# Performance work log

Hardware: AMD Instinct MI355X
Metric: run time of the kernel (lower is better)

## Reference

```python
import jax, jax.numpy as jnp
import numpy as np

D_MODEL = 1024
N_HEADS = 16
HEAD_DIM = D_MODEL // N_HEADS
ROPE_BASE = 10000.0


def setup_inputs() -> dict:
    key = jax.random.key(0)
    ks = jax.random.split(key, 5)
    B, S = 2, 2048
    x = jax.random.normal(ks[0], (B, S, D_MODEL), dtype=jnp.float32)
    scale = 1.0 / np.sqrt(D_MODEL)
    Wq = jax.random.normal(ks[1], (D_MODEL, D_MODEL), dtype=jnp.float32) * scale
    Wk = jax.random.normal(ks[2], (D_MODEL, D_MODEL), dtype=jnp.float32) * scale
    Wv = jax.random.normal(ks[3], (D_MODEL, D_MODEL), dtype=jnp.float32) * scale
    Wo = jax.random.normal(ks[4], (D_MODEL, D_MODEL), dtype=jnp.float32) * scale
    return {"x": x, "Wq": Wq, "Wk": Wk, "Wv": Wv, "Wo": Wo}


def _rope_cos_sin(seq_len, dtype):
    # inv_freq over half the head dim, duplicated (cat[freqs, freqs])
    inv_freq = 1.0 / (ROPE_BASE ** (jnp.arange(0, HEAD_DIM, 2, dtype=jnp.float32) / HEAD_DIM))
    t = jnp.arange(seq_len, dtype=jnp.float32)
    freqs = jnp.outer(t, inv_freq)                 # [S, HD/2]
    emb = jnp.concatenate([freqs, freqs], axis=-1)  # [S, HD]
    return jnp.cos(emb).astype(dtype), jnp.sin(emb).astype(dtype)


def _rotate_half(v):
    v1, v2 = jnp.split(v, 2, axis=-1)
    return jnp.concatenate([-v2, v1], axis=-1)


def reference(x, Wq, Wk, Wv, Wo):
    B, S, _ = x.shape
    # torch Linear: y = x @ W.T  (weights stored [out, in])
    def proj(W):
        y = jnp.einsum('bsd,ed->bse', x, W)
        return y.reshape(B, S, N_HEADS, HEAD_DIM).transpose(0, 2, 1, 3)  # [B,H,S,HD]
    q, k, v = proj(Wq), proj(Wk), proj(Wv)

    cos, sin = _rope_cos_sin(S, x.dtype)  # [S, HD]
    cos = cos[None, None]                 # [1,1,S,HD]
    sin = sin[None, None]
    q = q * cos + _rotate_half(q) * sin
    k = k * cos + _rotate_half(k) * sin

    scale = 1.0 / np.sqrt(HEAD_DIM)
    scores = jnp.einsum('bhqd,bhkd->bhqk', q, k) * scale  # [B,H,S,S]
    causal = jnp.triu(jnp.ones((S, S), dtype=bool), k=1)
    scores = jnp.where(causal, jnp.finfo(scores.dtype).min, scores)
    attn = jax.nn.softmax(scores, axis=-1)
    out = jnp.einsum('bhqk,bhkd->bhqd', attn, v)          # [B,H,S,HD]
    out = out.transpose(0, 2, 1, 3).reshape(B, S, D_MODEL)
    return jnp.einsum('bsd,ed->bse', out, Wo)
```

## Files before the change

### kernel.cpp

```cpp
#include <hip/hip_runtime.h>

typedef unsigned short u16;
typedef __attribute__((ext_vector_type(8))) short short8;
typedef __attribute__((ext_vector_type(4))) float floatx4;

#define D_MODEL 1024
#define NHEADS 16
#define HD 64
#define BATCH 2
#define SEQ 2048
#define MROWS (BATCH * SEQ)

static __device__ __forceinline__ u16 f2bf(float f) {
  unsigned int u = __float_as_uint(f);
  u += 0x7fffu + ((u >> 16) & 1u);
  return (u16)(u >> 16);
}

__global__ void cvt_all(const float* __restrict__ x, const float* __restrict__ wq,
                        const float* __restrict__ wk, const float* __restrict__ wv,
                        const float* __restrict__ wo, u16* __restrict__ xb,
                        u16* __restrict__ wqkvb, u16* __restrict__ wob) {
  const int i = blockIdx.x * 256 + threadIdx.x;
  const int chunk = i >> 18;
  const float* src;
  u16* dst;
  int loc;
  switch (chunk) {
    case 0: case 1: case 2: case 3: src = x;  dst = xb;              loc = i;              break;
    case 4:                          src = wq; dst = wqkvb;           loc = i - (4 << 18); break;
    case 5:                          src = wk; dst = wqkvb + 1048576; loc = i - (5 << 18); break;
    case 6:                          src = wv; dst = wqkvb + 2097152; loc = i - (6 << 18); break;
    default:                         src = wo; dst = wob;             loc = i - (7 << 18); break;
  }
  const float4 v = ((const float4*)src)[loc];
  ushort4 o;
  o.x = f2bf(v.x); o.y = f2bf(v.y); o.z = f2bf(v.z); o.w = f2bf(v.w);
  ((ushort4*)dst)[loc] = o;
}

__global__ __launch_bounds__(256) void gemm_qkv(
    const u16* __restrict__ A, const u16* __restrict__ B,
    u16* __restrict__ qb, u16* __restrict__ kb, u16* __restrict__ vb, int K) {
  __shared__ u16 As[2][128 * 32];
  __shared__ u16 Bs[2][128 * 32];
  const int t = threadIdx.x;
  const int lane = t & 63;
  const int wv = t >> 6;
  const int wr = wv >> 1, wc = wv & 1;
  const int m0 = blockIdx.y * 128, n0 = blockIdx.x * 128;
  const int qd = lane >> 4, lr = lane & 15;
  const int arow = lane >> 2;
  const int acol = (lane & 3) * 8;

  floatx4 acc[4][4];
#pragma unroll
  for (int i = 0; i < 4; ++i)
#pragma unroll
    for (int j = 0; j < 4; ++j) acc[i][j] = (floatx4){0.f, 0.f, 0.f, 0.f};

  for (int kt = 0; kt < K; kt += 64) {
    __syncthreads();
#pragma unroll
    for (int kh = 0; kh < 2; ++kh) {
#pragma unroll
      for (int i = 0; i < 2; ++i) {
        const int seg = wv * 2 + i;
        const u16* ga = &A[(size_t)(m0 + seg * 16 + arow) * K + kt + kh * 32 + acol];
        const u16* gb = &B[(size_t)(n0 + seg * 16 + arow) * K + kt + kh * 32 + acol];
        __builtin_amdgcn_global_load_lds(
            (const __attribute__((address_space(1))) void*)ga,
            (__attribute__((address_space(3))) void*)&As[kh][seg * 512], 16, 0, 0);
        __builtin_amdgcn_global_load_lds(
            (const __attribute__((address_space(1))) void*)gb,
            (__attribute__((address_space(3))) void*)&Bs[kh][seg * 512], 16, 0, 0);
      }
    }
    __syncthreads();

#pragma unroll
    for (int kh = 0; kh < 2; ++kh) {
      short8 af[4], bfr[4];
#pragma unroll
      for (int i = 0; i < 4; ++i)
        af[i] = *(const short8*)&As[kh][(wr * 64 + i * 16 + lr) * 32 + qd * 8];
#pragma unroll
      for (int j = 0; j < 4; ++j)
        bfr[j] = *(const short8*)&Bs[kh][(wc * 64 + j * 16 + lr) * 32 + qd * 8];
#pragma unroll
      for (int i = 0; i < 4; ++i)
#pragma unroll
        for (int j = 0; j < 4; ++j)
          acc[i][j] = __builtin_amdgcn_mfma_f32_16x16x32_bf16(af[i], bfr[j], acc[i][j], 0, 0, 0);
    }
  }

  const int tn = n0 >> 10;
  if (tn == 2) {
#pragma unroll
    for (int i = 0; i < 4; ++i) {
      const int mb = m0 + wr * 64 + i * 16 + qd * 4;
      const int b = mb >> 11, s = mb & 2047;
#pragma unroll
      for (int j = 0; j < 4; ++j) {
        const int nn = (n0 + wc * 64 + j * 16 + lr) & 1023;
        const int h = nn >> 6, d = nn & 63;
        ushort4 o;
        o.x = f2bf(acc[i][j][0]); o.y = f2bf(acc[i][j][1]);
        o.z = f2bf(acc[i][j][2]); o.w = f2bf(acc[i][j][3]);
        *(ushort4*)&vb[((size_t)(b * NHEADS + h) * HD + d) * SEQ + s] = o;
      }
    }
  } else {
    u16* dst = (tn == 0) ? qb : kb;
    const float qs = (tn == 0) ? 0.18033688011112042f : 1.0f;
    const int h = ((n0 & 1023) >> 6) + wc;
    const float inv0 = __builtin_exp2f(-(float)lr * 0.4152410118609203f);
    const float inv1 = __builtin_exp2f(-(float)(lr + 16) * 0.4152410118609203f);
#pragma unroll
    for (int i = 0; i < 4; ++i) {
      const int mb = m0 + wr * 64 + i * 16 + qd * 4;
      const int b = mb >> 11;
      const size_t rowbase = (size_t)(b * NHEADS + h) * SEQ;
#pragma unroll
      for (int r = 0; r < 4; ++r) {
        const int sq = (mb + r) & 2047;
        float s0, c0, s1, c1;
        __sincosf((float)sq * inv0, &s0, &c0);
        __sincosf((float)sq * inv1, &s1, &c1);
#pragma unroll
        for (int j = 0; j < 4; ++j) {
          const float v = acc[i][j][r];
          const float pv = acc[i][j ^ 2][r];
          const float cc = (j & 1) ? c1 : c0;
          const float ss = (j & 1) ? s1 : s0;
          const float res = (v * cc + ((j < 2) ? -pv : pv) * ss) * qs;
          dst[(rowbase + sq) * HD + j * 16 + lr] = f2bf(res);
        }
      }
    }
  }
}

__global__ __launch_bounds__(256) void gemm_out(
    const u16* __restrict__ A, const u16* __restrict__ B, float* __restrict__ fo,
    int N, int K) {
  __shared__ u16 As[2][64 * 32];
  __shared__ u16 Bs[2][64 * 32];
  const int t = threadIdx.x;
  const int lane = t & 63, wv = t >> 6;
  const int m0 = blockIdx.y * 64, n0 = blockIdx.x * 64;
  const int qd = lane >> 4, lr = lane & 15;
  const int arow = lane >> 2;
  const int acol = (lane & 3) * 8;

  floatx4 acc[4];
#pragma unroll
  for (int j = 0; j < 4; ++j) acc[j] = (floatx4){0.f, 0.f, 0.f, 0.f};

  for (int kt = 0; kt < K; kt += 64) {
    __syncthreads();
#pragma unroll
    for (int kh = 0; kh < 2; ++kh) {
      const u16* ga = &A[(size_t)(m0 + wv * 16 + arow) * K + kt + kh * 32 + acol];
      const u16* gb = &B[(size_t)(n0 + wv * 16 + arow) * K + kt + kh * 32 + acol];
      __builtin_amdgcn_global_load_lds(
          (const __attribute__((address_space(1))) void*)ga,
          (__attribute__((address_space(3))) void*)&As[kh][wv * 512], 16, 0, 0);
      __builtin_amdgcn_global_load_lds(
          (const __attribute__((address_space(1))) void*)gb,
          (__attribute__((address_space(3))) void*)&Bs[kh][wv * 512], 16, 0, 0);
    }
    __syncthreads();

#pragma unroll
    for (int kh = 0; kh < 2; ++kh) {
      const short8 af = *(const short8*)&As[kh][(wv * 16 + lr) * 32 + qd * 8];
#pragma unroll
      for (int j = 0; j < 4; ++j) {
        const short8 bfr = *(const short8*)&Bs[kh][(j * 16 + lr) * 32 + qd * 8];
        acc[j] = __builtin_amdgcn_mfma_f32_16x16x32_bf16(af, bfr, acc[j], 0, 0, 0);
      }
    }
  }
#pragma unroll
  for (int j = 0; j < 4; ++j)
#pragma unroll
    for (int r = 0; r < 4; ++r)
      fo[(size_t)(m0 + wv * 16 + qd * 4 + r) * N + n0 + j * 16 + lr] = acc[j][r];
}

__global__ __launch_bounds__(256, 2) void flash_mfma(
    const u16* __restrict__ Q, const u16* __restrict__ Kg,
    const u16* __restrict__ Vg, u16* __restrict__ O) {
  __shared__ u16 Ks[2][2][64 * 32];
  __shared__ u16 Vs[2][2][64 * 32];
  __shared__ u16 Ps[4][2][16][72];
  const int t = threadIdx.x;
  const int lane = t & 63, wv = t >> 6;
  const int lr = lane & 15, qd = lane >> 4;
  const int bh = blockIdx.x;
  const int y = (int)blockIdx.y;
  const int c = (y < 8) ? (15 - y) : (y - 8);
  const int nsteps = 2 * c + 2;
  const int q0w = c * 128 + wv * 32;
  const size_t baseQK = (size_t)bh * SEQ * HD;
  const size_t baseV = (size_t)bh * HD * SEQ;
  const int b = bh >> 4, h = bh & 15;
  const int srow = lane >> 2;
  const int scol = (lane & 3) * 8;

  auto stage = [&](int buf, int k0) {
    const int hh = wv & 1;
    if (wv < 2) {
#pragma unroll
      for (int seg = 0; seg < 4; ++seg) {
        const u16* g = &Kg[baseQK + (size_t)(k0 + seg * 16 + srow) * HD + hh * 32 + scol];
        __builtin_amdgcn_global_load_lds(
            (const __attribute__((address_space(1))) void*)g,
            (__attribute__((address_space(3))) void*)&Ks[buf][hh][seg * 512], 16, 0, 0);
      }
    } else {
#pragma unroll
      for (int seg = 0; seg < 4; ++seg) {
        const u16* g = &Vg[baseV + (size_t)(seg * 16 + srow) * SEQ + k0 + hh * 32 + scol];
        __builtin_amdgcn_global_load_lds(
            (const __attribute__((address_space(1))) void*)g,
            (__attribute__((address_space(3))) void*)&Vs[buf][hh][seg * 512], 16, 0, 0);
      }
    }
  };

  short8 qf[2][2];
#pragma unroll
  for (int i = 0; i < 2; ++i)
#pragma unroll
    for (int s = 0; s < 2; ++s)
      qf[i][s] = *(const short8*)&Q[baseQK + (size_t)(q0w + i * 16 + lr) * HD + s * 32 + qd * 8];

  float l_i[2] = {0.f, 0.f};
  floatx4 oacc[2][4];
#pragma unroll
  for (int i = 0; i < 2; ++i)
#pragma unroll
    for (int dj = 0; dj < 4; ++dj) oacc[i][dj] = (floatx4){0.f, 0.f, 0.f, 0.f};

  stage(0, 0);

  for (int kt = 0; kt < nsteps; ++kt) {
    __syncthreads();
    if (kt + 1 < nsteps) stage((kt + 1) & 1, (kt + 1) * 64);
    const int k0 = kt * 64;
    if (k0 > q0w + 31) continue;
    const int buf = kt & 1;

    short8 kf[2][4], vf[2][4];
#pragma unroll
    for (int s = 0; s < 2; ++s)
#pragma unroll
      for (int jj = 0; jj < 4; ++jj)
        kf[s][jj] = *(const short8*)&Ks[buf][s][(jj * 16 + lr) * 32 + qd * 8];
#pragma unroll
    for (int s = 0; s < 2; ++s)
#pragma unroll
      for (int dj = 0; dj < 4; ++dj)
        vf[s][dj] = *(const short8*)&Vs[buf][s][(dj * 16 + lr) * 32 + qd * 8];

    floatx4 sv[2][4];
#pragma unroll
    for (int i = 0; i < 2; ++i)
#pragma unroll
      for (int jj = 0; jj < 4; ++jj) sv[i][jj] = (floatx4){0.f, 0.f, 0.f, 0.f};
#pragma unroll
    for (int s = 0; s < 2; ++s)
#pragma unroll
      for (int jj = 0; jj < 4; ++jj) {
        sv[1][jj] = __builtin_amdgcn_mfma_f32_16x16x32_bf16(kf[s][jj], qf[1][s], sv[1][jj], 0, 0, 0);
        sv[0][jj] = __builtin_amdgcn_mfma_f32_16x16x32_bf16(kf[s][jj], qf[0][s], sv[0][jj], 0, 0, 0);
      }

#pragma unroll
    for (int i = 0; i < 2; ++i) {
      const int dq = (q0w + i * 16) - k0;
      if (dq < 63) {
#pragma unroll
        for (int jj = 0; jj < 4; ++jj)
#pragma unroll
          for (int r = 0; r < 4; ++r)
            if (jj * 16 + qd * 4 + r > dq + lr) sv[i][jj][r] = -1e30f;
      }
      float rs = 0.f;
#pragma unroll
      for (int jj = 0; jj < 4; ++jj) {
        const float p0 = __builtin_exp2f(sv[i][jj][0]);
        const float p1 = __builtin_exp2f(sv[i][jj][1]);
        const float p2 = __builtin_exp2f(sv[i][jj][2]);
        const float p3 = __builtin_exp2f(sv[i][jj][3]);
        rs += (p0 + p1) + (p2 + p3);
        uint2 pk;
        pk.x = __builtin_amdgcn_perm(__float_as_uint(p1), __float_as_uint(p0), 0x07060302);
        pk.y = __builtin_amdgcn_perm(__float_as_uint(p3), __float_as_uint(p2), 0x07060302);
        *(uint2*)&Ps[wv][i][lr][jj * 16 + qd * 4] = pk;
      }
      l_i[i] += rs;
    }

#pragma unroll
    for (int i = 0; i < 2; ++i) {
      const short8 pf0 = *(const short8*)&Ps[wv][i][lr][qd * 8];
      const short8 pf1 = *(const short8*)&Ps[wv][i][lr][32 + qd * 8];
#pragma unroll
      for (int dj = 0; dj < 4; ++dj)
        oacc[i][dj] = __builtin_amdgcn_mfma_f32_16x16x32_bf16(pf0, vf[0][dj], oacc[i][dj], 0, 0, 0);
#pragma unroll
      for (int dj = 0; dj < 4; ++dj)
        oacc[i][dj] = __builtin_amdgcn_mfma_f32_16x16x32_bf16(pf1, vf[1][dj], oacc[i][dj], 0, 0, 0);
    }
  }

#pragma unroll
  for (int i = 0; i < 2; ++i) {
    float lf = l_i[i];
    lf += __shfl_xor(lf, 16, 64);
    lf += __shfl_xor(lf, 32, 64);
#pragma unroll
    for (int r = 0; r < 4; ++r) {
      const float linv = 1.f / __shfl(lf, qd * 4 + r, 64);
      const int q = q0w + i * 16 + qd * 4 + r;
#pragma unroll
      for (int dj = 0; dj < 4; ++dj)
        O[(size_t)(b * SEQ + q) * D_MODEL + h * HD + dj * 16 + lr] = f2bf(oacc[i][dj][r] * linv);
    }
  }
}

extern "C" void kernel_launch(void* const* d_in, const int* in_sizes, int n_in,
                              void* d_out, int out_size, void* d_ws, size_t ws_size,
                              hipStream_t stream) {
  const float* x  = (const float*)d_in[0];
  const float* Wq = (const float*)d_in[1];
  const float* Wk = (const float*)d_in[2];
  const float* Wv = (const float*)d_in[3];
  const float* Wo = (const float*)d_in[4];
  float* out = (float*)d_out;

  u16* xb = (u16*)d_ws;
  u16* wqkv = xb + 4194304;
  u16* wo = wqkv + 3145728;
  u16* qb = wo + 1048576;
  u16* kb = qb + 4194304;
  u16* vb = kb + 4194304;
  u16* ow = vb + 4194304;

  cvt_all<<<8192, 256, 0, stream>>>(x, Wq, Wk, Wv, Wo, xb, wqkv, wo);
  gemm_qkv<<<dim3(24, 32), 256, 0, stream>>>(xb, wqkv, qb, kb, vb, 1024);
  flash_mfma<<<dim3(32, 16), 256, 0, stream>>>(qb, kb, vb, ow);
  gemm_out<<<dim3(16, 64), 256, 0, stream>>>(ow, wo, out, 1024, 1024);
}
```

Measured before the change: 180.6 us.

## Split flash attention block across 8 waves with 16 query rows each

The attention kernel now runs 512 threads per block (8 waves), and each wave handles 16 query rows instead of 32. K/V staging is spread so every wave issues one K and one V async load per tile. The aim is more wave-level parallelism and latency hiding per CU, with fewer registers per wave. The cost is that each K/V fragment loaded from LDS now feeds half as many MFMAs, so LDS read traffic per FLOP doubles, and there are more threads per barrier.

```diff
diff --git a/kernel.cpp b/kernel.cpp
--- a/kernel.cpp
+++ b/kernel.cpp
@@ -190,12 +190,12 @@
       fo[(size_t)(m0 + wv * 16 + qd * 4 + r) * N + n0 + j * 16 + lr] = acc[j][r];
 }
 
-__global__ __launch_bounds__(256, 2) void flash_mfma(
+__global__ __launch_bounds__(512, 4) void flash_mfma(
     const u16* __restrict__ Q, const u16* __restrict__ Kg,
     const u16* __restrict__ Vg, u16* __restrict__ O) {
   __shared__ u16 Ks[2][2][64 * 32];
   __shared__ u16 Vs[2][2][64 * 32];
-  __shared__ u16 Ps[4][2][16][72];
+  __shared__ u16 Ps[8][16][72];
   const int t = threadIdx.x;
   const int lane = t & 63, wv = t >> 6;
   const int lr = lane & 15, qd = lane >> 4;
@@ -203,47 +203,35 @@
   const int y = (int)blockIdx.y;
   const int c = (y < 8) ? (15 - y) : (y - 8);
   const int nsteps = 2 * c + 2;
-  const int q0w = c * 128 + wv * 32;
+  const int q0w = c * 128 + wv * 16;
   const size_t baseQK = (size_t)bh * SEQ * HD;
   const size_t baseV = (size_t)bh * HD * SEQ;
   const int b = bh >> 4, h = bh & 15;
   const int srow = lane >> 2;
   const int scol = (lane & 3) * 8;
+  const int shh = (wv >> 2) & 1;
+  const int sseg = wv & 3;
 
   auto stage = [&](int buf, int k0) {
-    const int hh = wv & 1;
-    if (wv < 2) {
-#pragma unroll
-      for (int seg = 0; seg < 4; ++seg) {
-        const u16* g = &Kg[baseQK + (size_t)(k0 + seg * 16 + srow) * HD + hh * 32 + scol];
-        __builtin_amdgcn_global_load_lds(
-            (const __attribute__((address_space(1))) void*)g,
-            (__attribute__((address_space(3))) void*)&Ks[buf][hh][seg * 512], 16, 0, 0);
-      }
-    } else {
-#pragma unroll
-      for (int seg = 0; seg < 4; ++seg) {
-        const u16* g = &Vg[baseV + (size_t)(seg * 16 + srow) * SEQ + k0 + hh * 32 + scol];
-        __builtin_amdgcn_global_load_lds(
-            (const __attribute__((address_space(1))) void*)g,
-            (__attribute__((address_space(3))) void*)&Vs[buf][hh][seg * 512], 16, 0, 0);
-      }
-    }
+    const u16* gk = &Kg[baseQK + (size_t)(k0 + sseg * 16 + srow) * HD + shh * 32 + scol];
+    __builtin_amdgcn_global_load_lds(
+        (const __attribute__((address_space(1))) void*)gk,
+        (__attribute__((address_space(3))) void*)&Ks[buf][shh][sseg * 512], 16, 0, 0);
+    const u16* gv = &Vg[baseV + (size_t)(sseg * 16 + srow) * SEQ + k0 + shh * 32 + scol];
+    __builtin_amdgcn_global_load_lds(
+        (const __attribute__((address_space(1))) void*)gv,
+        (__attribute__((address_space(3))) void*)&Vs[buf][shh][sseg * 512], 16, 0, 0);
   };
 
-  short8 qf[2][2];
-#pragma unroll
-  for (int i = 0; i < 2; ++i)
-#pragma unroll
-    for (int s = 0; s < 2; ++s)
-      qf[i][s] = *(const short8*)&Q[baseQK + (size_t)(q0w + i * 16 + lr) * HD + s * 32 + qd * 8];
-
-  float l_i[2] = {0.f, 0.f};
-  floatx4 oacc[2][4];
-#pragma unroll
-  for (int i = 0; i < 2; ++i)
-#pragma unroll
-    for (int dj = 0; dj < 4; ++dj) oacc[i][dj] = (floatx4){0.f, 0.f, 0.f, 0.f};
+  short8 qf[2];
+#pragma unroll
+  for (int s = 0; s < 2; ++s)
+    qf[s] = *(const short8*)&Q[baseQK + (size_t)(q0w + lr) * HD + s * 32 + qd * 8];
+
+  float l_i = 0.f;
+  floatx4 oacc[4];
+#pragma unroll
+  for (int dj = 0; dj < 4; ++dj) oacc[dj] = (floatx4){0.f, 0.f, 0.f, 0.f};
 
   stage(0, 0);
 
@@ -251,7 +239,7 @@
     __syncthreads();
     if (kt + 1 < nsteps) stage((kt + 1) & 1, (kt + 1) * 64);
     const int k0 = kt * 64;
-    if (k0 > q0w + 31) continue;
+    if (k0 > q0w + 15) continue;
     const int buf = kt & 1;
 
     short8 kf[2][4], vf[2][4];
@@ -266,70 +254,60 @@
       for (int dj = 0; dj < 4; ++dj)
         vf[s][dj] = *(const short8*)&Vs[buf][s][(dj * 16 + lr) * 32 + qd * 8];
 
-    floatx4 sv[2][4];
-#pragma unroll
-    for (int i = 0; i < 2; ++i)
-#pragma unroll
-      for (int jj = 0; jj < 4; ++jj) sv[i][jj] = (floatx4){0.f, 0.f, 0.f, 0.f};
+    floatx4 sv[4];
+#pragma unroll
+    for (int jj = 0; jj < 4; ++jj) sv[jj] = (floatx4){0.f, 0.f, 0.f, 0.f};
 #pragma unroll
     for (int s = 0; s < 2; ++s)
 #pragma unroll
-      for (int jj = 0; jj < 4; ++jj) {
-        sv[1][jj] = __builtin_amdgcn_mfma_f32_16x16x32_bf16(kf[s][jj], qf[1][s], sv[1][jj], 0, 0, 0);
-        sv[0][jj] = __builtin_amdgcn_mfma_f32_16x16x32_bf16(kf[s][jj], qf[0][s], sv[0][jj], 0, 0, 0);
-      }
-
-#pragma unroll
-    for (int i = 0; i < 2; ++i) {
-      const int dq = (q0w + i * 16) - k0;
-      if (dq < 63) {
-#pragma unroll
-        for (int jj = 0; jj < 4; ++jj)
-#pragma unroll
-          for (int r = 0; r < 4; ++r)
-            if (jj * 16 + qd * 4 + r > dq + lr) sv[i][jj][r] = -1e30f;
-      }
-      float rs = 0.f;
-#pragma unroll
-      for (int jj = 0; jj < 4; ++jj) {
-        const float p0 = __builtin_exp2f(sv[i][jj][0]);
-        const float p1 = __builtin_exp2f(sv[i][jj][1]);
-        const float p2 = __builtin_exp2f(sv[i][jj][2]);
-        const float p3 = __builtin_exp2f(sv[i][jj][3]);
-        rs += (p0 + p1) + (p2 + p3);
-        uint2 pk;
-        pk.x = __builtin_amdgcn_perm(__float_as_uint(p1), __float_as_uint(p0), 0x07060302);
-        pk.y = __builtin_amdgcn_perm(__float_as_uint(p3), __float_as_uint(p2), 0x07060302);
-        *(uint2*)&Ps[wv][i][lr][jj * 16 + qd * 4] = pk;
-      }
-      l_i[i] += rs;
-    }
-
-#pragma unroll
-    for (int i = 0; i < 2; ++i) {
-      const short8 pf0 = *(const short8*)&Ps[wv][i][lr][qd * 8];
-      const short8 pf1 = *(const short8*)&Ps[wv][i][lr][32 + qd * 8];
-#pragma unroll
-      for (int dj = 0; dj < 4; ++dj)
-        oacc[i][dj] = __builtin_amdgcn_mfma_f32_16x16x32_bf16(pf0, vf[0][dj], oacc[i][dj], 0, 0, 0);
-#pragma unroll
-      for (int dj = 0; dj < 4; ++dj)
-        oacc[i][dj] = __builtin_amdgcn_mfma_f32_16x16x32_bf16(pf1, vf[1][dj], oacc[i][dj], 0, 0, 0);
-    }
-  }
-
-#pragma unroll
-  for (int i = 0; i < 2; ++i) {
-    float lf = l_i[i];
+      for (int jj = 0; jj < 4; ++jj)
+        sv[jj] = __builtin_amdgcn_mfma_f32_16x16x32_bf16(kf[s][jj], qf[s], sv[jj], 0, 0, 0);
+
+    const int dq = q0w - k0;
+    if (dq < 63) {
+#pragma unroll
+      for (int jj = 0; jj < 4; ++jj)
+#pragma unroll
+        for (int r = 0; r < 4; ++r)
+          if (jj * 16 + qd * 4 + r > dq + lr) sv[jj][r] = -1e30f;
+    }
+
+    float rs = 0.f;
+#pragma unroll
+    for (int jj = 0; jj < 4; ++jj) {
+      const float p0 = __builtin_exp2f(sv[jj][0]);
+      const float p1 = __builtin_exp2f(sv[jj][1]);
+      const float p2 = __builtin_exp2f(sv[jj][2]);
+      const float p3 = __builtin_exp2f(sv[jj][3]);
+      rs += (p0 + p1) + (p2 + p3);
+      uint2 pk;
+      pk.x = __builtin_amdgcn_perm(__float_as_uint(p1), __float_as_uint(p0), 0x07060302);
+      pk.y = __builtin_amdgcn_perm(__float_as_uint(p3), __float_as_uint(p2), 0x07060302);
+      *(uint2*)&Ps[wv][lr][jj * 16 + qd * 4] = pk;
+    }
+    l_i += rs;
+
+    const short8 pf0 = *(const short8*)&Ps[wv][lr][qd * 8];
+    const short8 pf1 = *(const short8*)&Ps[wv][lr][32 + qd * 8];
+#pragma unroll
+    for (int dj = 0; dj < 4; ++dj)
+      oacc[dj] = __builtin_amdgcn_mfma_f32_16x16x32_bf16(pf0, vf[0][dj], oacc[dj], 0, 0, 0);
+#pragma unroll
+    for (int dj = 0; dj < 4; ++dj)
+      oacc[dj] = __builtin_amdgcn_mfma_f32_16x16x32_bf16(pf1, vf[1][dj], oacc[dj], 0, 0, 0);
+  }
+
+  {
+    float lf = l_i;
     lf += __shfl_xor(lf, 16, 64);
     lf += __shfl_xor(lf, 32, 64);
 #pragma unroll
     for (int r = 0; r < 4; ++r) {
       const float linv = 1.f / __shfl(lf, qd * 4 + r, 64);
-      const int q = q0w + i * 16 + qd * 4 + r;
+      const int q = q0w + qd * 4 + r;
 #pragma unroll
       for (int dj = 0; dj < 4; ++dj)
-        O[(size_t)(b * SEQ + q) * D_MODEL + h * HD + dj * 16 + lr] = f2bf(oacc[i][dj][r] * linv);
+        O[(size_t)(b * SEQ + q) * D_MODEL + h * HD + dj * 16 + lr] = f2bf(oacc[dj][r] * linv);
     }
   }
 }
@@ -354,6 +332,6 @@
 
   cvt_all<<<8192, 256, 0, stream>>>(x, Wq, Wk, Wv, Wo, xb, wqkv, wo);
   gemm_qkv<<<dim3(24, 32), 256, 0, stream>>>(xb, wqkv, qb, kb, vb, 1024);
-  flash_mfma<<<dim3(32, 16), 256, 0, stream>>>(qb, kb, vb, ow);
+  flash_mfma<<<dim3(32, 16), 512, 0, stream>>>(qb, kb, vb, ow);
   gemm_out<<<dim3(16, 64), 256, 0, stream>>>(ow, wo, out, 1024, 1024);
 }
```

Result: no change. 182.4 us (+1.0%).

## Stage 128-key chunks per barrier in flash attention and shrink P buffer

Applied to the files above, without the earlier changes.

The flash attention loop now stages two 64-key sub-tiles (128 keys) per double-buffered step, so there is half as many __syncthreads and stage calls per query block. The K/V LDS buffers double in size. To offset that, the per-wave P scratch is cut from two query sub-tiles to one, reused by writing and reading P inside each i iteration. Costs are more LDS per block (about 68KB), which may limit the two-blocks-per-CU occupancy, a possible LDS hazard from reusing Ps across i without a barrier, and wasted loads on causal-tail sub-tiles that are skipped.

```diff
diff --git a/kernel.cpp b/kernel.cpp
--- a/kernel.cpp
+++ b/kernel.cpp
@@ -15,6 +15,12 @@
   unsigned int u = __float_as_uint(f);
   u += 0x7fffu + ((u >> 16) & 1u);
   return (u16)(u >> 16);
+}
+
+static __device__ __forceinline__ void glds16(const u16* g, u16* l) {
+  __builtin_amdgcn_global_load_lds(
+      (const __attribute__((address_space(1))) void*)g,
+      (__attribute__((address_space(3))) void*)l, 16, 0, 0);
 }
 
 __global__ void cvt_all(const float* __restrict__ x, const float* __restrict__ wq,
@@ -66,14 +72,8 @@
 #pragma unroll
       for (int i = 0; i < 2; ++i) {
         const int seg = wv * 2 + i;
-        const u16* ga = &A[(size_t)(m0 + seg * 16 + arow) * K + kt + kh * 32 + acol];
-        const u16* gb = &B[(size_t)(n0 + seg * 16 + arow) * K + kt + kh * 32 + acol];
-        __builtin_amdgcn_global_load_lds(
-            (const __attribute__((address_space(1))) void*)ga,
-            (__attribute__((address_space(3))) void*)&As[kh][seg * 512], 16, 0, 0);
-        __builtin_amdgcn_global_load_lds(
-            (const __attribute__((address_space(1))) void*)gb,
-            (__attribute__((address_space(3))) void*)&Bs[kh][seg * 512], 16, 0, 0);
+        glds16(&A[(size_t)(m0 + seg * 16 + arow) * K + kt + kh * 32 + acol], &As[kh][seg * 512]);
+        glds16(&B[(size_t)(n0 + seg * 16 + arow) * K + kt + kh * 32 + acol], &Bs[kh][seg * 512]);
       }
     }
     __syncthreads();
@@ -162,14 +162,8 @@
     __syncthreads();
 #pragma unroll
     for (int kh = 0; kh < 2; ++kh) {
-      const u16* ga = &A[(size_t)(m0 + wv * 16 + arow) * K + kt + kh * 32 + acol];
-      const u16* gb = &B[(size_t)(n0 + wv * 16 + arow) * K + kt + kh * 32 + acol];
-      __builtin_amdgcn_global_load_lds(
-          (const __attribute__((address_space(1))) void*)ga,
-          (__attribute__((address_space(3))) void*)&As[kh][wv * 512], 16, 0, 0);
-      __builtin_amdgcn_global_load_lds(
-          (const __attribute__((address_space(1))) void*)gb,
-          (__attribute__((address_space(3))) void*)&Bs[kh][wv * 512], 16, 0, 0);
+      glds16(&A[(size_t)(m0 + wv * 16 + arow) * K + kt + kh * 32 + acol], &As[kh][wv * 512]);
+      glds16(&B[(size_t)(n0 + wv * 16 + arow) * K + kt + kh * 32 + acol], &Bs[kh][wv * 512]);
     }
     __syncthreads();
 
@@ -193,16 +187,16 @@
 __global__ __launch_bounds__(256, 2) void flash_mfma(
     const u16* __restrict__ Q, const u16* __restrict__ Kg,
     const u16* __restrict__ Vg, u16* __restrict__ O) {
-  __shared__ u16 Ks[2][2][64 * 32];
-  __shared__ u16 Vs[2][2][64 * 32];
-  __shared__ u16 Ps[4][2][16][72];
+  __shared__ u16 Ks[2][2][2][64 * 32];
+  __shared__ u16 Vs[2][2][2][64 * 32];
+  __shared__ u16 Ps[4][16][72];
   const int t = threadIdx.x;
   const int lane = t & 63, wv = t >> 6;
   const int lr = lane & 15, qd = lane >> 4;
   const int bh = blockIdx.x;
   const int y = (int)blockIdx.y;
   const int c = (y < 8) ? (15 - y) : (y - 8);
-  const int nsteps = 2 * c + 2;
+  const int nst2 = c + 1;
   const int q0w = c * 128 + wv * 32;
   const size_t baseQK = (size_t)bh * SEQ * HD;
   const size_t baseV = (size_t)bh * HD * SEQ;
@@ -211,23 +205,22 @@
   const int scol = (lane & 3) * 8;
 
   auto stage = [&](int buf, int k0) {
-    const int hh = wv & 1;
     if (wv < 2) {
-#pragma unroll
-      for (int seg = 0; seg < 4; ++seg) {
-        const u16* g = &Kg[baseQK + (size_t)(k0 + seg * 16 + srow) * HD + hh * 32 + scol];
-        __builtin_amdgcn_global_load_lds(
-            (const __attribute__((address_space(1))) void*)g,
-            (__attribute__((address_space(3))) void*)&Ks[buf][hh][seg * 512], 16, 0, 0);
-      }
+      const int sub = wv;
+#pragma unroll
+      for (int hh = 0; hh < 2; ++hh)
+#pragma unroll
+        for (int seg = 0; seg < 4; ++seg)
+          glds16(&Kg[baseQK + (size_t)(k0 + sub * 64 + seg * 16 + srow) * HD + hh * 32 + scol],
+                 &Ks[buf][sub][hh][seg * 512]);
     } else {
-#pragma unroll
-      for (int seg = 0; seg < 4; ++seg) {
-        const u16* g = &Vg[baseV + (size_t)(seg * 16 + srow) * SEQ + k0 + hh * 32 + scol];
-        __builtin_amdgcn_global_load_lds(
-            (const __attribute__((address_space(1))) void*)g,
-            (__attribute__((address_space(3))) void*)&Vs[buf][hh][seg * 512], 16, 0, 0);
-      }
+      const int sub = wv - 2;
+#pragma unroll
+      for (int hh = 0; hh < 2; ++hh)
+#pragma unroll
+        for (int seg = 0; seg < 4; ++seg)
+          glds16(&Vg[baseV + (size_t)(seg * 16 + srow) * SEQ + k0 + sub * 64 + hh * 32 + scol],
+                 &Vs[buf][sub][hh][seg * 512]);
     }
   };
 
@@ -247,74 +240,75 @@
 
   stage(0, 0);
 
-  for (int kt = 0; kt < nsteps; ++kt) {
-    __syncthreads();
-    if (kt + 1 < nsteps) stage((kt + 1) & 1, (kt + 1) * 64);
-    const int k0 = kt * 64;
-    if (k0 > q0w + 31) continue;
-    const int buf = kt & 1;
-
-    short8 kf[2][4], vf[2][4];
-#pragma unroll
-    for (int s = 0; s < 2; ++s)
-#pragma unroll
-      for (int jj = 0; jj < 4; ++jj)
-        kf[s][jj] = *(const short8*)&Ks[buf][s][(jj * 16 + lr) * 32 + qd * 8];
-#pragma unroll
-    for (int s = 0; s < 2; ++s)
-#pragma unroll
-      for (int dj = 0; dj < 4; ++dj)
-        vf[s][dj] = *(const short8*)&Vs[buf][s][(dj * 16 + lr) * 32 + qd * 8];
-
-    floatx4 sv[2][4];
-#pragma unroll
-    for (int i = 0; i < 2; ++i)
-#pragma unroll
-      for (int jj = 0; jj < 4; ++jj) sv[i][jj] = (floatx4){0.f, 0.f, 0.f, 0.f};
-#pragma unroll
-    for (int s = 0; s < 2; ++s)
-#pragma unroll
-      for (int jj = 0; jj < 4; ++jj) {
-        sv[1][jj] = __builtin_amdgcn_mfma_f32_16x16x32_bf16(kf[s][jj], qf[1][s], sv[1][jj], 0, 0, 0);
-        sv[0][jj] = __builtin_amdgcn_mfma_f32_16x16x32_bf16(kf[s][jj], qf[0][s], sv[0][jj], 0, 0, 0);
-      }
-
-#pragma unroll
-    for (int i = 0; i < 2; ++i) {
-      const int dq = (q0w + i * 16) - k0;
-      if (dq < 63) {
+  for (int kt2 = 0; kt2 < nst2; ++kt2) {
+    __syncthreads();
+    if (kt2 + 1 < nst2) stage((kt2 + 1) & 1, (kt2 + 1) * 128);
+    const int buf = kt2 & 1;
+
+#pragma unroll
+    for (int sub = 0; sub < 2; ++sub) {
+      const int k0 = kt2 * 128 + sub * 64;
+      if (k0 > q0w + 31) continue;
+
+      short8 kf[2][4], vf[2][4];
+#pragma unroll
+      for (int s = 0; s < 2; ++s)
 #pragma unroll
         for (int jj = 0; jj < 4; ++jj)
-#pragma unroll
-          for (int r = 0; r < 4; ++r)
-            if (jj * 16 + qd * 4 + r > dq + lr) sv[i][jj][r] = -1e30f;
-      }
-      float rs = 0.f;
-#pragma unroll
-      for (int jj = 0; jj < 4; ++jj) {
-        const float p0 = __builtin_exp2f(sv[i][jj][0]);
-        const float p1 = __builtin_exp2f(sv[i][jj][1]);
-        const float p2 = __builtin_exp2f(sv[i][jj][2]);
-        const float p3 = __builtin_exp2f(sv[i][jj][3]);
-        rs += (p0 + p1) + (p2 + p3);
-        uint2 pk;
-        pk.x = __builtin_amdgcn_perm(__float_as_uint(p1), __float_as_uint(p0), 0x07060302);
-        pk.y = __builtin_amdgcn_perm(__float_as_uint(p3), __float_as_uint(p2), 0x07060302);
-        *(uint2*)&Ps[wv][i][lr][jj * 16 + qd * 4] = pk;
-      }
-      l_i[i] += rs;
-    }
-
-#pragma unroll
-    for (int i = 0; i < 2; ++i) {
-      const short8 pf0 = *(const short8*)&Ps[wv][i][lr][qd * 8];
-      const short8 pf1 = *(const short8*)&Ps[wv][i][lr][32 + qd * 8];
-#pragma unroll
-      for (int dj = 0; dj < 4; ++dj)
-        oacc[i][dj] = __builtin_amdgcn_mfma_f32_16x16x32_bf16(pf0, vf[0][dj], oacc[i][dj], 0, 0, 0);
-#pragma unroll
-      for (int dj = 0; dj < 4; ++dj)
-        oacc[i][dj] = __builtin_amdgcn_mfma_f32_16x16x32_bf16(pf1, vf[1][dj], oacc[i][dj], 0, 0, 0);
+          kf[s][jj] = *(const short8*)&Ks[buf][sub][s][(jj * 16 + lr) * 32 + qd * 8];
+#pragma unroll
+      for (int s = 0; s < 2; ++s)
+#pragma unroll
+        for (int dj = 0; dj < 4; ++dj)
+          vf[s][dj] = *(const short8*)&Vs[buf][sub][s][(dj * 16 + lr) * 32 + qd * 8];
+
+      floatx4 sv[2][4];
+#pragma unroll
+      for (int i = 0; i < 2; ++i)
+#pragma unroll
+        for (int jj = 0; jj < 4; ++jj) sv[i][jj] = (floatx4){0.f, 0.f, 0.f, 0.f};
+#pragma unroll
+      for (int s = 0; s < 2; ++s)
+#pragma unroll
+        for (int jj = 0; jj < 4; ++jj) {
+          sv[1][jj] = __builtin_amdgcn_mfma_f32_16x16x32_bf16(kf[s][jj], qf[1][s], sv[1][jj], 0, 0, 0);
+          sv[0][jj] = __builtin_amdgcn_mfma_f32_16x16x32_bf16(kf[s][jj], qf[0][s], sv[0][jj], 0, 0, 0);
+        }
+
+#pragma unroll
+      for (int i = 0; i < 2; ++i) {
+        const int dq = (q0w + i * 16) - k0;
+        if (dq < 63) {
+#pragma unroll
+          for (int jj = 0; jj < 4; ++jj)
+#pragma unroll
+            for (int r = 0; r < 4; ++r)
+              if (jj * 16 + qd * 4 + r > dq + lr) sv[i][jj][r] = -1e30f;
+        }
+        float rs = 0.f;
+#pragma unroll
+        for (int jj = 0; jj < 4; ++jj) {
+          const float p0 = __builtin_exp2f(sv[i][jj][0]);
+          const float p1 = __builtin_exp2f(sv[i][jj][1]);
+          const float p2 = __builtin_exp2f(sv[i][jj][2]);
+          const float p3 = __builtin_exp2f(sv[i][jj][3]);
+          rs += (p0 + p1) + (p2 + p3);
+          uint2 pk;
+          pk.x = __builtin_amdgcn_perm(__float_as_uint(p1), __float_as_uint(p0), 0x07060302);
+          pk.y = __builtin_amdgcn_perm(__float_as_uint(p3), __float_as_uint(p2), 0x07060302);
+          *(uint2*)&Ps[wv][lr][jj * 16 + qd * 4] = pk;
+        }
+        l_i[i] += rs;
+
+        const short8 pf0 = *(const short8*)&Ps[wv][lr][qd * 8];
+        const short8 pf1 = *(const short8*)&Ps[wv][lr][32 + qd * 8];
+#pragma unroll
+        for (int dj = 0; dj < 4; ++dj)
+          oacc[i][dj] = __builtin_amdgcn_mfma_f32_16x16x32_bf16(pf0, vf[0][dj], oacc[i][dj], 0, 0, 0);
+#pragma unroll
+        for (int dj = 0; dj < 4; ++dj)
+          oacc[i][dj] = __builtin_amdgcn_mfma_f32_16x16x32_bf16(pf1, vf[1][dj], oacc[i][dj], 0, 0, 0);
+      }
     }
   }
 
```

Measured after the change: 177.3 us. Within noise of the previous version (-1.8%).
